# Kernel optimization log

Measured on AMD Instinct MI355X. Metric: run time of the kernel, lower is better.

Reference implementation:

```python
import jax, jax.numpy as jnp
import numpy as np

LN2 = float(np.log(2.0))
N_ATOMS = 100_000
N_PAIRS = 2_000_000
F = 64     # number_of_atom_features
R = 16     # number_of_radial_basis_functions
N_RES = 3


def setup_inputs() -> dict:
    key = jax.random.key(0)
    ks = jax.random.split(key, 16)
    s = 0.05
    inp = {
        "pair_indices": jax.random.randint(ks[0], (2, N_PAIRS), 0, N_ATOMS, dtype=jnp.int32),
        "f_ij": jax.random.normal(ks[1], (N_PAIRS, 1, R), dtype=jnp.float32),
        "d_ij": jax.random.uniform(ks[2], (N_PAIRS, 1), dtype=jnp.float32),
        "atomic_embedding": jax.random.normal(ks[3], (N_ATOMS, F), dtype=jnp.float32),
        # AttentionMask parameter G: [F, R]
        "G": jax.random.normal(ks[4], (F, R), dtype=jnp.float32),
        # interaction_i / interaction_j linear layers (stored as [in, out])
        "Wi": jax.random.normal(ks[5], (F, F), dtype=jnp.float32) * s,
        "bi": jnp.zeros((F,), dtype=jnp.float32),
        "Wj": jax.random.normal(ks[6], (F, F), dtype=jnp.float32) * s,
        "bj": jnp.zeros((F,), dtype=jnp.float32),
        # residual blocks, stacked over N_RES
        "res_W1": jax.random.normal(ks[7], (N_RES, F, F), dtype=jnp.float32) * s,
        "res_b1": jnp.zeros((N_RES, F), dtype=jnp.float32),
        "res_W2": jax.random.normal(ks[8], (N_RES, F, F), dtype=jnp.float32) * s,
        "res_b2": jnp.zeros((N_RES, F), dtype=jnp.float32),
        # process_v linear
        "Wv": jax.random.normal(ks[9], (F, F), dtype=jnp.float32) * s,
        "bv": jnp.zeros((F,), dtype=jnp.float32),
    }
    return inp


def reference(pair_indices, f_ij, d_ij, atomic_embedding,
              G, Wi, bi, Wj, bj, res_W1, res_b1, res_W2, res_b2, Wv, bv):
    idx_i, idx_j = pair_indices[0], pair_indices[1]
    f = f_ij.squeeze(1)                                  # [P, R]

    # ShiftedSoftplus on node embeddings
    x = jax.nn.softplus(atomic_embedding) - LN2          # [N, F]

    x_i_prime = jax.nn.softplus(x @ Wi + bi)             # [N, F]
    x_j_prime = jax.nn.softplus(x[idx_j] @ Wj + bj)      # [P, F] (gather)
    f_prime = f @ G.T                                    # [P, F] attention mask

    msg = x_j_prime * f_prime                            # [P, F]
    summed = jax.ops.segment_sum(msg, idx_i, num_segments=atomic_embedding.shape[0])

    v = x_i_prime + summed                               # [N, F]
    for l in range(res_W1.shape[0]):
        h = jax.nn.softplus(v @ res_W1[l] + res_b1[l])
        v = v + (h @ res_W2[l] + res_b2[l])
    return jax.nn.softplus(v) @ Wv + bv
```

## Files before the change

### kernel.cpp

```cpp
#include <hip/hip_runtime.h>
#include <math.h>

#define FDIM 64
#define RDIM 16
#define LN2F 0.69314718055994530942f
#define LTS 68
#define NBINR 14336
#define NCHUNK 64

typedef __bf16 bf8_t __attribute__((ext_vector_type(8)));
typedef float  f4_t  __attribute__((ext_vector_type(4)));

__device__ __forceinline__ float sp(float x) {
    return fmaxf(x, 0.0f) + __logf(1.0f + __expf(-fabsf(x)));
}

__global__ __launch_bounds__(256) void k_prep(
    const float* s0, const float* s1, const float* s2, const float* s3,
    const float* s4, const float* s5, const float* s6, const float* s7,
    const float* s8, __bf16* __restrict__ dst)
{
    const float* srcs[9] = {s0, s1, s2, s3, s4, s5, s6, s7, s8};
    const float* W = srcs[blockIdx.x];
    __bf16* d = dst + (size_t)blockIdx.x * 4096;
    for (int slot = threadIdx.x; slot < 512; slot += 256) {
        int f = slot >> 6, l = slot & 63;
        int kt = f >> 2, nt = f & 3;
        int row0 = kt * 32 + (l >> 4) * 8;
        int col = nt * 16 + (l & 15);
#pragma unroll
        for (int j = 0; j < 8; ++j)
            d[slot * 8 + j] = (__bf16)W[(row0 + j) * FDIM + col];
    }
}

__global__ __launch_bounds__(256) void k_hist2(
    const int* __restrict__ idx_i, int* __restrict__ Cmat,
    int P, int N, int nRange)
{
    __shared__ int h[NBINR];
    const int chunk = blockIdx.x / nRange;
    const int range = blockIdx.x % nRange;
    const int lo = range * NBINR;
    const int nb = min(NBINR, N - lo);
    for (int u = threadIdx.x; u < NBINR; u += 256) h[u] = 0;
    __syncthreads();

    const int chunkSz = (P + NCHUNK - 1) / NCHUNK;
    const int cs = chunk * chunkSz;
    const int ce = min(P, cs + chunkSz);
    int p = cs + threadIdx.x;
    for (; p + 768 < ce; p += 1024) {
        int i0 = idx_i[p];
        int i1 = idx_i[p + 256];
        int i2 = idx_i[p + 512];
        int i3 = idx_i[p + 768];
        unsigned u0 = (unsigned)(i0 - lo);
        unsigned u1 = (unsigned)(i1 - lo);
        unsigned u2 = (unsigned)(i2 - lo);
        unsigned u3 = (unsigned)(i3 - lo);
        if (u0 < (unsigned)nb) atomicAdd(&h[u0], 1);
        if (u1 < (unsigned)nb) atomicAdd(&h[u1], 1);
        if (u2 < (unsigned)nb) atomicAdd(&h[u2], 1);
        if (u3 < (unsigned)nb) atomicAdd(&h[u3], 1);
    }
    for (; p < ce; p += 256) {
        unsigned u = (unsigned)(idx_i[p] - lo);
        if (u < (unsigned)nb) atomicAdd(&h[u], 1);
    }
    __syncthreads();
    for (int u = threadIdx.x; u < nb; u += 256)
        Cmat[(size_t)chunk * N + lo + u] = h[u];
}

__global__ __launch_bounds__(256) void k_scanR(
    int* __restrict__ Cmat, int* __restrict__ tot, int N)
{
    const int bA = blockIdx.x * 512 + threadIdx.x;
    const int bB = bA + 256;
    const bool okA = bA < N, okB = bB < N;
    int runA = 0, runB = 0;
    for (int c = 0; c < NCHUNK; ++c) {
        const size_t base = (size_t)c * N;
        if (okA) { int val = Cmat[base + bA]; Cmat[base + bA] = runA; runA += val; }
        if (okB) { int val = Cmat[base + bB]; Cmat[base + bB] = runB; runB += val; }
    }
    if (okA) tot[bA] = runA;
    if (okB) tot[bB] = runB;
}

__device__ __forceinline__ void tile_in(float* T, const float* __restrict__ src,
                                        int a0, int rows, int lane)
{
#pragma unroll 4
    for (int i = 0; i < 16; ++i) {
        int r = i * 4 + (lane >> 4);
        int col = (lane & 15) * 4;
        float4 val = make_float4(0.f, 0.f, 0.f, 0.f);
        if (r < rows) val = *(const float4*)&src[(size_t)(a0 + r) * FDIM + col];
        *(float4*)&T[r * LTS + col] = val;
    }
}

__device__ __forceinline__ void build_a(const float* T, int lane, bool actLn2,
                                        bf8_t (&aF)[4][2])
{
    const int l15 = lane & 15, quad = lane >> 4;
#pragma unroll
    for (int mt = 0; mt < 4; ++mt) {
#pragma unroll
        for (int kt = 0; kt < 2; ++kt) {
            const float* rp = &T[(mt * 16 + l15) * LTS + kt * 32 + quad * 8];
            float4 u0 = *(const float4*)rp;
            float4 u1 = *(const float4*)(rp + 4);
            float e[8] = {u0.x, u0.y, u0.z, u0.w, u1.x, u1.y, u1.z, u1.w};
            bf8_t f;
#pragma unroll
            for (int j = 0; j < 8; ++j) {
                float t = actLn2 ? (sp(e[j]) - LN2F) : e[j];
                f[j] = (__bf16)t;
            }
            aF[mt][kt] = f;
        }
    }
}

__global__ __launch_bounds__(256) void k_atoms(
    const float* __restrict__ emb, const __bf16* __restrict__ wf,
    const float* __restrict__ bi, const float* __restrict__ bj,
    float* __restrict__ v, float* __restrict__ y, int N)
{
    __shared__ float tile[4][64 * LTS];
    const int lane = threadIdx.x & 63;
    const int wv = threadIdx.x >> 6;
    float* T = tile[wv];
    const int l15 = lane & 15, quad = lane >> 4;

    const bf8_t* wiF = (const bf8_t*)wf;
    const bf8_t* wjF = (const bf8_t*)(wf + 4096);
    bf8_t wi[2][4], wj[2][4];
#pragma unroll
    for (int kt = 0; kt < 2; ++kt)
#pragma unroll
        for (int nt = 0; nt < 4; ++nt) {
            wi[kt][nt] = wiF[(kt * 4 + nt) * 64 + lane];
            wj[kt][nt] = wjF[(kt * 4 + nt) * 64 + lane];
        }
    float biv[4], bjv[4];
#pragma unroll
    for (int nt = 0; nt < 4; ++nt) {
        biv[nt] = bi[nt * 16 + l15];
        bjv[nt] = bj[nt * 16 + l15];
    }

    const int nTiles = (N + 63) >> 6;
    for (int t = blockIdx.x * 4 + wv; t < nTiles; t += gridDim.x * 4) {
        const int a0 = t << 6;
        const int rows = min(64, N - a0);
        tile_in(T, emb, a0, rows, lane);
        bf8_t aF[4][2];
        build_a(T, lane, true, aF);
#pragma unroll
        for (int mt = 0; mt < 4; ++mt)
#pragma unroll
            for (int nt = 0; nt < 4; ++nt) {
                f4_t acc = {biv[nt], biv[nt], biv[nt], biv[nt]};
                acc = __builtin_amdgcn_mfma_f32_16x16x32_bf16(aF[mt][0], wi[0][nt], acc, 0, 0, 0);
                acc = __builtin_amdgcn_mfma_f32_16x16x32_bf16(aF[mt][1], wi[1][nt], acc, 0, 0, 0);
#pragma unroll
                for (int reg = 0; reg < 4; ++reg) {
                    int r = mt * 16 + quad * 4 + reg;
                    if (r < rows) v[(size_t)(a0 + r) * FDIM + nt * 16 + l15] = sp(acc[reg]);
                }
            }
#pragma unroll
        for (int mt = 0; mt < 4; ++mt)
#pragma unroll
            for (int nt = 0; nt < 4; ++nt) {
                f4_t acc = {bjv[nt], bjv[nt], bjv[nt], bjv[nt]};
                acc = __builtin_amdgcn_mfma_f32_16x16x32_bf16(aF[mt][0], wj[0][nt], acc, 0, 0, 0);
                acc = __builtin_amdgcn_mfma_f32_16x16x32_bf16(aF[mt][1], wj[1][nt], acc, 0, 0, 0);
#pragma unroll
                for (int reg = 0; reg < 4; ++reg) {
                    int r = mt * 16 + quad * 4 + reg;
                    if (r < rows) y[(size_t)(a0 + r) * FDIM + nt * 16 + l15] = sp(acc[reg]);
                }
            }
    }
}

__global__ __launch_bounds__(256) void k_post(
    const __bf16* __restrict__ wf,
    const float* __restrict__ rb1, const float* __restrict__ rb2,
    const float* __restrict__ bv,
    float* __restrict__ v, int N)
{
    __shared__ float tile[4][64 * LTS];
    const int lane = threadIdx.x & 63;
    const int wv = threadIdx.x >> 6;
    float* T = tile[wv];
    const int l15 = lane & 15, quad = lane >> 4;

    float b1v[3][4], b2v[3][4], bvv[4];
#pragma unroll
    for (int l = 0; l < 3; ++l)
#pragma unroll
        for (int nt = 0; nt < 4; ++nt) {
            b1v[l][nt] = rb1[l * FDIM + nt * 16 + l15];
            b2v[l][nt] = rb2[l * FDIM + nt * 16 + l15];
        }
#pragma unroll
    for (int nt = 0; nt < 4; ++nt) bvv[nt] = bv[nt * 16 + l15];

    const int nTiles = (N + 63) >> 6;
    for (int t = blockIdx.x * 4 + wv; t < nTiles; t += gridDim.x * 4) {
        const int a0 = t << 6;
        const int rows = min(64, N - a0);
        tile_in(T, v, a0, rows, lane);
        float vC[16][4];
#pragma unroll
        for (int mt = 0; mt < 4; ++mt)
#pragma unroll
            for (int nt = 0; nt < 4; ++nt)
#pragma unroll
                for (int reg = 0; reg < 4; ++reg)
                    vC[mt * 4 + nt][reg] =
                        T[(mt * 16 + quad * 4 + reg) * LTS + nt * 16 + l15];

        for (int l = 0; l < 3; ++l) {
            const bf8_t* w1f = (const bf8_t*)(wf + (size_t)(2 * l) * 4096);
            const bf8_t* w2f = (const bf8_t*)(wf + (size_t)(2 * l + 1) * 4096);
            bf8_t aF[4][2];
            build_a(T, lane, false, aF);
#pragma unroll
            for (int mt = 0; mt < 4; ++mt)
#pragma unroll
                for (int nt = 0; nt < 4; ++nt) {
                    f4_t acc = {b1v[l][nt], b1v[l][nt], b1v[l][nt], b1v[l][nt]};
                    acc = __builtin_amdgcn_mfma_f32_16x16x32_bf16(aF[mt][0], w1f[(0 * 4 + nt) * 64 + lane], acc, 0, 0, 0);
                    acc = __builtin_amdgcn_mfma_f32_16x16x32_bf16(aF[mt][1], w1f[(1 * 4 + nt) * 64 + lane], acc, 0, 0, 0);
#pragma unroll
                    for (int reg = 0; reg < 4; ++reg)
                        T[(mt * 16 + quad * 4 + reg) * LTS + nt * 16 + l15] = sp(acc[reg]);
                }
            bf8_t hF[4][2];
            build_a(T, lane, false, hF);
#pragma unroll
            for (int mt = 0; mt < 4; ++mt)
#pragma unroll
                for (int nt = 0; nt < 4; ++nt) {
                    f4_t acc = {b2v[l][nt], b2v[l][nt], b2v[l][nt], b2v[l][nt]};
                    acc = __builtin_amdgcn_mfma_f32_16x16x32_bf16(hF[mt][0], w2f[(0 * 4 + nt) * 64 + lane], acc, 0, 0, 0);
                    acc = __builtin_amdgcn_mfma_f32_16x16x32_bf16(hF[mt][1], w2f[(1 * 4 + nt) * 64 + lane], acc, 0, 0, 0);
#pragma unroll
                    for (int reg = 0; reg < 4; ++reg)
                        vC[mt * 4 + nt][reg] += acc[reg];
                }
            if (l < 2) {
#pragma unroll
                for (int mt = 0; mt < 4; ++mt)
#pragma unroll
                    for (int nt = 0; nt < 4; ++nt)
#pragma unroll
                        for (int reg = 0; reg < 4; ++reg)
                            T[(mt * 16 + quad * 4 + reg) * LTS + nt * 16 + l15] =
                                vC[mt * 4 + nt][reg];
            }
        }
#pragma unroll
        for (int mt = 0; mt < 4; ++mt)
#pragma unroll
            for (int nt = 0; nt < 4; ++nt)
#pragma unroll
                for (int reg = 0; reg < 4; ++reg)
                    T[(mt * 16 + quad * 4 + reg) * LTS + nt * 16 + l15] =
                        sp(vC[mt * 4 + nt][reg]);
        bf8_t fF[4][2];
        build_a(T, lane, false, fF);
        const bf8_t* wvf = (const bf8_t*)(wf + (size_t)6 * 4096);
#pragma unroll
        for (int mt = 0; mt < 4; ++mt)
#pragma unroll
            for (int nt = 0; nt < 4; ++nt) {
                f4_t acc = {bvv[nt], bvv[nt], bvv[nt], bvv[nt]};
                acc = __builtin_amdgcn_mfma_f32_16x16x32_bf16(fF[mt][0], wvf[(0 * 4 + nt) * 64 + lane], acc, 0, 0, 0);
                acc = __builtin_amdgcn_mfma_f32_16x16x32_bf16(fF[mt][1], wvf[(1 * 4 + nt) * 64 + lane], acc, 0, 0, 0);
#pragma unroll
                for (int reg = 0; reg < 4; ++reg) {
                    int r = mt * 16 + quad * 4 + reg;
                    if (r < rows) v[(size_t)(a0 + r) * FDIM + nt * 16 + l15] = acc[reg];
                }
            }
    }
}

__global__ __launch_bounds__(256) void k_scan_a(
    const int* __restrict__ cnt, int* __restrict__ part, int N)
{
    __shared__ int red[256];
    int b = blockIdx.x, t = threadIdx.x;
    int base = b * 1024 + t * 4;
    int s = 0;
#pragma unroll
    for (int i = 0; i < 4; ++i) { int a = base + i; if (a < N) s += cnt[a]; }
    red[t] = s; __syncthreads();
    for (int off = 128; off > 0; off >>= 1) {
        if (t < off) red[t] += red[t + off];
        __syncthreads();
    }
    if (t == 0) part[b] = red[0];
}

__global__ __launch_bounds__(256) void k_scan_b(int* __restrict__ part, int nPart)
{
    __shared__ int lds[256];
    int t = threadIdx.x;
    int base = t * 4;
    int v[4]; int s = 0;
#pragma unroll
    for (int i = 0; i < 4; ++i) { v[i] = (base + i < nPart) ? part[base + i] : 0; s += v[i]; }
    lds[t] = s; __syncthreads();
    int run = s;
    for (int off = 1; off < 256; off <<= 1) {
        int x = (t >= off) ? lds[t - off] : 0;
        __syncthreads();
        lds[t] += x;
        __syncthreads();
    }
    int excl = lds[t] - run;
#pragma unroll
    for (int i = 0; i < 4; ++i) { if (base + i < nPart) { part[base + i] = excl; excl += v[i]; } }
}

__global__ __launch_bounds__(256) void k_scan_c(
    const int* __restrict__ cnt, const int* __restrict__ part,
    int* __restrict__ start, int N, int P)
{
    __shared__ int lds[256];
    int b = blockIdx.x, t = threadIdx.x;
    int base = b * 1024 + t * 4;
    int v[4]; int s = 0;
#pragma unroll
    for (int i = 0; i < 4; ++i) { int a = base + i; v[i] = (a < N) ? cnt[a] : 0; s += v[i]; }
    lds[t] = s; __syncthreads();
    int run = s;
    for (int off = 1; off < 256; off <<= 1) {
        int x = (t >= off) ? lds[t - off] : 0;
        __syncthreads();
        lds[t] += x;
        __syncthreads();
    }
    int pre = part[b] + (lds[t] - run);
#pragma unroll
    for (int i = 0; i < 4; ++i) {
        int a = base + i;
        if (a < N) { start[a] = pre; pre += v[i]; }
    }
    if (b == 0 && t == 0) start[N] = P;
}

__global__ __launch_bounds__(256) void k_scatter2(
    const int* __restrict__ pidx, const int* __restrict__ Cmat,
    const int* __restrict__ start, int2* __restrict__ sorted,
    int P, int N, int nRange)
{
    __shared__ int cur[NBINR];
    const int chunk = blockIdx.x / nRange;
    const int range = blockIdx.x % nRange;
    const int lo = range * NBINR;
    const int nb = min(NBINR, N - lo);
    for (int u = threadIdx.x; u < nb; u += 256)
        cur[u] = start[lo + u] + Cmat[(size_t)chunk * N + lo + u];
    __syncthreads();

    const int chunkSz = (P + NCHUNK - 1) / NCHUNK;
    const int cs = chunk * chunkSz;
    const int ce = min(P, cs + chunkSz);
    int p = cs + threadIdx.x;
    for (; p + 768 < ce; p += 1024) {
        int i0 = pidx[p];
        int i1 = pidx[p + 256];
        int i2 = pidx[p + 512];
        int i3 = pidx[p + 768];
        int j0 = pidx[P + p];
        int j1 = pidx[P + p + 256];
        int j2 = pidx[P + p + 512];
        int j3 = pidx[P + p + 768];
        unsigned u0 = (unsigned)(i0 - lo);
        unsigned u1 = (unsigned)(i1 - lo);
        unsigned u2 = (unsigned)(i2 - lo);
        unsigned u3 = (unsigned)(i3 - lo);
        if (u0 < (unsigned)nb) { int pos = atomicAdd(&cur[u0], 1); sorted[pos] = make_int2(p, j0); }
        if (u1 < (unsigned)nb) { int pos = atomicAdd(&cur[u1], 1); sorted[pos] = make_int2(p + 256, j1); }
        if (u2 < (unsigned)nb) { int pos = atomicAdd(&cur[u2], 1); sorted[pos] = make_int2(p + 512, j2); }
        if (u3 < (unsigned)nb) { int pos = atomicAdd(&cur[u3], 1); sorted[pos] = make_int2(p + 768, j3); }
    }
    for (; p < ce; p += 256) {
        int i = pidx[p];
        unsigned u = (unsigned)(i - lo);
        if (u < (unsigned)nb) {
            int j = pidx[P + p];
            int pos = atomicAdd(&cur[u], 1);
            sorted[pos] = make_int2(p, j);
        }
    }
}

__global__ __launch_bounds__(256) void k_seg(
    const int2* __restrict__ sorted, const int* __restrict__ start,
    const float* __restrict__ f_ij, const float* __restrict__ G,
    const float* __restrict__ y, float* __restrict__ v, int N)
{
    const int c = threadIdx.x & 63;
    const int w = __builtin_amdgcn_readfirstlane((blockIdx.x << 2) | (threadIdx.x >> 6));
    const int nw = gridDim.x << 2;

    float g[16];
    {
        const float4* gp = (const float4*)(G + c * RDIM);
        float4 g0 = gp[0], g1 = gp[1], g2 = gp[2], g3 = gp[3];
        g[0] = g0.x;  g[1] = g0.y;  g[2] = g0.z;  g[3] = g0.w;
        g[4] = g1.x;  g[5] = g1.y;  g[6] = g1.z;  g[7] = g1.w;
        g[8] = g2.x;  g[9] = g2.y;  g[10] = g2.z; g[11] = g2.w;
        g[12] = g3.x; g[13] = g3.y; g[14] = g3.z; g[15] = g3.w;
    }

    for (int a = w; a < N; a += nw) {
        const int s = start[a], e = start[a + 1];
        float vold = v[(size_t)a * FDIM + c];
        float t[16];
#pragma unroll
        for (int r = 0; r < 16; ++r) t[r] = 0.0f;

        for (int base = s; base < e; base += 64) {
            const int nn = (e - base < 64) ? (e - base) : 64;
            const int li = (c < nn) ? c : (nn - 1);
            const int2 E = sorted[base + li];
            const int pk = E.x, jk = E.y;

            int k = 0;
            for (; k + 8 <= nn; k += 8) {
                int pp[8], jj[8];
#pragma unroll
                for (int u = 0; u < 8; ++u) {
                    pp[u] = __builtin_amdgcn_readlane(pk, k + u);
                    jj[u] = __builtin_amdgcn_readlane(jk, k + u);
                }
                float yv[8];
#pragma unroll
                for (int u = 0; u < 8; ++u)
                    yv[u] = y[(size_t)jj[u] * FDIM + c];
#pragma unroll
                for (int u = 0; u < 8; ++u) {
                    const float* f = f_ij + (size_t)pp[u] * RDIM;
#pragma unroll
                    for (int r = 0; r < 16; ++r) t[r] = fmaf(f[r], yv[u], t[r]);
                }
            }
            for (; k + 4 <= nn; k += 4) {
                int pp[4], jj[4];
#pragma unroll
                for (int u = 0; u < 4; ++u) {
                    pp[u] = __builtin_amdgcn_readlane(pk, k + u);
                    jj[u] = __builtin_amdgcn_readlane(jk, k + u);
                }
                float yv[4];
#pragma unroll
                for (int u = 0; u < 4; ++u)
                    yv[u] = y[(size_t)jj[u] * FDIM + c];
#pragma unroll
                for (int u = 0; u < 4; ++u) {
                    const float* f = f_ij + (size_t)pp[u] * RDIM;
#pragma unroll
                    for (int r = 0; r < 16; ++r) t[r] = fmaf(f[r], yv[u], t[r]);
                }
            }
            for (; k < nn; ++k) {
                const int p0 = __builtin_amdgcn_readlane(pk, k);
                const int j0 = __builtin_amdgcn_readlane(jk, k);
                float y0 = y[(size_t)j0 * FDIM + c];
                const float* f0 = f_ij + (size_t)p0 * RDIM;
#pragma unroll
                for (int r = 0; r < 16; ++r) t[r] = fmaf(f0[r], y0, t[r]);
            }
        }

        float acc0 = 0.f, acc1 = 0.f, acc2 = 0.f, acc3 = 0.f;
#pragma unroll
        for (int r = 0; r < 16; r += 4) {
            acc0 = fmaf(g[r + 0], t[r + 0], acc0);
            acc1 = fmaf(g[r + 1], t[r + 1], acc1);
            acc2 = fmaf(g[r + 2], t[r + 2], acc2);
            acc3 = fmaf(g[r + 3], t[r + 3], acc3);
        }
        v[(size_t)a * FDIM + c] = vold + (acc0 + acc1) + (acc2 + acc3);
    }
}

extern "C" void kernel_launch(void* const* d_in, const int* in_sizes, int n_in,
                              void* d_out, int out_size, void* d_ws, size_t ws_size,
                              hipStream_t stream)
{
    const int*   pidx = (const int*)d_in[0];
    const float* f_ij = (const float*)d_in[1];
    const float* emb  = (const float*)d_in[3];
    const float* G    = (const float*)d_in[4];
    const float* Wi   = (const float*)d_in[5];
    const float* bi   = (const float*)d_in[6];
    const float* Wj   = (const float*)d_in[7];
    const float* bj   = (const float*)d_in[8];
    const float* rW1  = (const float*)d_in[9];
    const float* rb1  = (const float*)d_in[10];
    const float* rW2  = (const float*)d_in[11];
    const float* rb2  = (const float*)d_in[12];
    const float* Wv   = (const float*)d_in[13];
    const float* bv   = (const float*)d_in[14];

    const int P = in_sizes[0] / 2;
    const int N = in_sizes[3] / FDIM;

    float* v = (float*)d_out;

    char* ws = (char*)d_ws;
    size_t off = 0;
    float*  y      = (float*)(ws + off);
    int*    Cmat   = (int*)(ws + off);    off += (size_t)N * FDIM * 4;
    int*    tot    = (int*)(ws + off);    off += (size_t)N * 4;
    int*    start  = (int*)(ws + off);    off += (size_t)(N + 1) * 4;
    off = (off + 15) & ~(size_t)15;
    int*    part   = (int*)(ws + off);    off += (size_t)4096 * 4;
    off = (off + 15) & ~(size_t)15;
    int2*   sorted = (int2*)(ws + off);   off += (size_t)P * 8;
    off = (off + 15) & ~(size_t)15;
    __bf16* wf     = (__bf16*)(ws + off); off += (size_t)9 * 4096 * 2;

    const int nRange = (N + NBINR - 1) / NBINR;
    const int nPart = (N + 1023) / 1024;
    const int nTiles = (N + 63) >> 6;
    const int gTiles = (nTiles + 3) / 4;

    dim3 blk(256);
    k_prep<<<9, blk, 0, stream>>>(Wi, Wj, rW1, rW2, rW1 + 4096, rW2 + 4096,
                                  rW1 + 8192, rW2 + 8192, Wv, wf);
    k_hist2<<<NCHUNK * nRange, blk, 0, stream>>>(pidx, Cmat, P, N, nRange);
    k_scanR<<<(N + 511) / 512, blk, 0, stream>>>(Cmat, tot, N);
    k_scan_a<<<nPart, blk, 0, stream>>>(tot, part, N);
    k_scan_b<<<1, blk, 0, stream>>>(part, nPart);
    k_scan_c<<<nPart, blk, 0, stream>>>(tot, part, start, N, P);
    k_scatter2<<<NCHUNK * nRange, blk, 0, stream>>>(pidx, Cmat, start, sorted, P, N, nRange);
    k_atoms<<<gTiles, blk, 0, stream>>>(emb, wf, bi, bj, v, y, N);
    k_seg<<<4096, blk, 0, stream>>>(sorted, start, f_ij, G, y, v, N);
    k_post<<<gTiles, blk, 0, stream>>>(wf + (size_t)2 * 4096, rb1, rb2, bv, v, N);
}
```

Baseline: 634.3 us.

## Pre-sort f_ij as fp16 during scatter and use fdot2 in segment kernel

The scatter kernel now writes each pair's radial features, converted to fp16, into the sorted order alongside its j index. The segment kernel can then read them contiguously instead of gathering f_ij rows at random. The segment kernel computes each pair's f·G dot product with packed fp16 dot2 instructions per channel, replacing the 16-wide accumulation followed by a G reduction. This trades extra per-channel dot work and fp16 precision loss for coalesced, halved f traffic. It also drops the 4x-unrolled scatter loop, and the scatter now has to read all f_ij in random-write order.

```diff
diff --git a/kernel.cpp b/kernel.cpp
--- a/kernel.cpp
+++ b/kernel.cpp
@@ -10,9 +10,18 @@
 
 typedef __bf16 bf8_t __attribute__((ext_vector_type(8)));
 typedef float  f4_t  __attribute__((ext_vector_type(4)));
+typedef _Float16 h2_t __attribute__((ext_vector_type(2)));
 
 __device__ __forceinline__ float sp(float x) {
     return fmaxf(x, 0.0f) + __logf(1.0f + __expf(-fabsf(x)));
+}
+
+__device__ __forceinline__ float fdot2f(h2_t a, h2_t b, float c) {
+#if __has_builtin(__builtin_amdgcn_fdot2)
+    return __builtin_amdgcn_fdot2(a, b, c, false);
+#else
+    return c + (float)a[0] * (float)b[0] + (float)a[1] * (float)b[1];
+#endif
 }
 
 __global__ __launch_bounds__(256) void k_prep(
@@ -360,8 +369,9 @@
 }
 
 __global__ __launch_bounds__(256) void k_scatter2(
-    const int* __restrict__ pidx, const int* __restrict__ Cmat,
-    const int* __restrict__ start, int2* __restrict__ sorted,
+    const int* __restrict__ pidx, const float* __restrict__ f_ij,
+    const int* __restrict__ Cmat, const int* __restrict__ start,
+    int* __restrict__ sortedJ, _Float16* __restrict__ sortedF,
     int P, int N, int nRange)
 {
     __shared__ int cur[NBINR];
@@ -376,123 +386,100 @@
     const int chunkSz = (P + NCHUNK - 1) / NCHUNK;
     const int cs = chunk * chunkSz;
     const int ce = min(P, cs + chunkSz);
-    int p = cs + threadIdx.x;
-    for (; p + 768 < ce; p += 1024) {
-        int i0 = pidx[p];
-        int i1 = pidx[p + 256];
-        int i2 = pidx[p + 512];
-        int i3 = pidx[p + 768];
-        int j0 = pidx[P + p];
-        int j1 = pidx[P + p + 256];
-        int j2 = pidx[P + p + 512];
-        int j3 = pidx[P + p + 768];
-        unsigned u0 = (unsigned)(i0 - lo);
-        unsigned u1 = (unsigned)(i1 - lo);
-        unsigned u2 = (unsigned)(i2 - lo);
-        unsigned u3 = (unsigned)(i3 - lo);
-        if (u0 < (unsigned)nb) { int pos = atomicAdd(&cur[u0], 1); sorted[pos] = make_int2(p, j0); }
-        if (u1 < (unsigned)nb) { int pos = atomicAdd(&cur[u1], 1); sorted[pos] = make_int2(p + 256, j1); }
-        if (u2 < (unsigned)nb) { int pos = atomicAdd(&cur[u2], 1); sorted[pos] = make_int2(p + 512, j2); }
-        if (u3 < (unsigned)nb) { int pos = atomicAdd(&cur[u3], 1); sorted[pos] = make_int2(p + 768, j3); }
-    }
-    for (; p < ce; p += 256) {
+    for (int p = cs + threadIdx.x; p < ce; p += 256) {
         int i = pidx[p];
         unsigned u = (unsigned)(i - lo);
         if (u < (unsigned)nb) {
             int j = pidx[P + p];
             int pos = atomicAdd(&cur[u], 1);
-            sorted[pos] = make_int2(p, j);
+            sortedJ[pos] = j;
+            const float4* fp = (const float4*)(f_ij + (size_t)p * RDIM);
+            float4 A = fp[0], B = fp[1], C4 = fp[2], D = fp[3];
+            h2_t hv[8];
+            hv[0] = h2_t{(_Float16)A.x, (_Float16)A.y};
+            hv[1] = h2_t{(_Float16)A.z, (_Float16)A.w};
+            hv[2] = h2_t{(_Float16)B.x, (_Float16)B.y};
+            hv[3] = h2_t{(_Float16)B.z, (_Float16)B.w};
+            hv[4] = h2_t{(_Float16)C4.x, (_Float16)C4.y};
+            hv[5] = h2_t{(_Float16)C4.z, (_Float16)C4.w};
+            hv[6] = h2_t{(_Float16)D.x, (_Float16)D.y};
+            hv[7] = h2_t{(_Float16)D.z, (_Float16)D.w};
+            _Float16* dst = sortedF + (size_t)pos * 16;
+            *(uint4*)dst = *(const uint4*)&hv[0];
+            *(uint4*)(dst + 8) = *(const uint4*)&hv[4];
         }
     }
 }
 
 __global__ __launch_bounds__(256) void k_seg(
-    const int2* __restrict__ sorted, const int* __restrict__ start,
-    const float* __restrict__ f_ij, const float* __restrict__ G,
+    const int* __restrict__ sortedJ, const _Float16* __restrict__ sortedF,
+    const int* __restrict__ start, const float* __restrict__ G,
     const float* __restrict__ y, float* __restrict__ v, int N)
 {
     const int c = threadIdx.x & 63;
     const int w = __builtin_amdgcn_readfirstlane((blockIdx.x << 2) | (threadIdx.x >> 6));
     const int nw = gridDim.x << 2;
 
-    float g[16];
+    h2_t g2[8];
     {
         const float4* gp = (const float4*)(G + c * RDIM);
-        float4 g0 = gp[0], g1 = gp[1], g2 = gp[2], g3 = gp[3];
-        g[0] = g0.x;  g[1] = g0.y;  g[2] = g0.z;  g[3] = g0.w;
-        g[4] = g1.x;  g[5] = g1.y;  g[6] = g1.z;  g[7] = g1.w;
-        g[8] = g2.x;  g[9] = g2.y;  g[10] = g2.z; g[11] = g2.w;
-        g[12] = g3.x; g[13] = g3.y; g[14] = g3.z; g[15] = g3.w;
+        float4 g0 = gp[0], g1 = gp[1], g2v = gp[2], g3 = gp[3];
+        g2[0] = h2_t{(_Float16)g0.x, (_Float16)g0.y};
+        g2[1] = h2_t{(_Float16)g0.z, (_Float16)g0.w};
+        g2[2] = h2_t{(_Float16)g1.x, (_Float16)g1.y};
+        g2[3] = h2_t{(_Float16)g1.z, (_Float16)g1.w};
+        g2[4] = h2_t{(_Float16)g2v.x, (_Float16)g2v.y};
+        g2[5] = h2_t{(_Float16)g2v.z, (_Float16)g2v.w};
+        g2[6] = h2_t{(_Float16)g3.x, (_Float16)g3.y};
+        g2[7] = h2_t{(_Float16)g3.z, (_Float16)g3.w};
     }
 
     for (int a = w; a < N; a += nw) {
-        const int s = start[a], e = start[a + 1];
+        const int s = __builtin_amdgcn_readfirstlane(start[a]);
+        const int e = __builtin_amdgcn_readfirstlane(start[a + 1]);
         float vold = v[(size_t)a * FDIM + c];
-        float t[16];
-#pragma unroll
-        for (int r = 0; r < 16; ++r) t[r] = 0.0f;
+        float acc0 = 0.f, acc1 = 0.f, acc2 = 0.f, acc3 = 0.f;
 
         for (int base = s; base < e; base += 64) {
             const int nn = (e - base < 64) ? (e - base) : 64;
             const int li = (c < nn) ? c : (nn - 1);
-            const int2 E = sorted[base + li];
-            const int pk = E.x, jk = E.y;
+            const int jkv = sortedJ[base + li];
 
             int k = 0;
             for (; k + 8 <= nn; k += 8) {
-                int pp[8], jj[8];
-#pragma unroll
-                for (int u = 0; u < 8; ++u) {
-                    pp[u] = __builtin_amdgcn_readlane(pk, k + u);
-                    jj[u] = __builtin_amdgcn_readlane(jk, k + u);
-                }
+                int jj[8];
+#pragma unroll
+                for (int u = 0; u < 8; ++u)
+                    jj[u] = __builtin_amdgcn_readlane(jkv, k + u);
                 float yv[8];
 #pragma unroll
                 for (int u = 0; u < 8; ++u)
                     yv[u] = y[(size_t)jj[u] * FDIM + c];
+                const h2_t* f2 = (const h2_t*)(sortedF + (size_t)(base + k) * 16);
 #pragma unroll
                 for (int u = 0; u < 8; ++u) {
-                    const float* f = f_ij + (size_t)pp[u] * RDIM;
-#pragma unroll
-                    for (int r = 0; r < 16; ++r) t[r] = fmaf(f[r], yv[u], t[r]);
+                    float d = 0.f;
+#pragma unroll
+                    for (int r = 0; r < 8; ++r)
+                        d = fdot2f(f2[u * 8 + r], g2[r], d);
+                    if ((u & 3) == 0) acc0 = fmaf(d, yv[u], acc0);
+                    else if ((u & 3) == 1) acc1 = fmaf(d, yv[u], acc1);
+                    else if ((u & 3) == 2) acc2 = fmaf(d, yv[u], acc2);
+                    else acc3 = fmaf(d, yv[u], acc3);
                 }
             }
-            for (; k + 4 <= nn; k += 4) {
-                int pp[4], jj[4];
-#pragma unroll
-                for (int u = 0; u < 4; ++u) {
-                    pp[u] = __builtin_amdgcn_readlane(pk, k + u);
-                    jj[u] = __builtin_amdgcn_readlane(jk, k + u);
-                }
-                float yv[4];
-#pragma unroll
-                for (int u = 0; u < 4; ++u)
-                    yv[u] = y[(size_t)jj[u] * FDIM + c];
-#pragma unroll
-                for (int u = 0; u < 4; ++u) {
-                    const float* f = f_ij + (size_t)pp[u] * RDIM;
-#pragma unroll
-                    for (int r = 0; r < 16; ++r) t[r] = fmaf(f[r], yv[u], t[r]);
-                }
-            }
             for (; k < nn; ++k) {
-                const int p0 = __builtin_amdgcn_readlane(pk, k);
-                const int j0 = __builtin_amdgcn_readlane(jk, k);
+                const int j0 = __builtin_amdgcn_readlane(jkv, k);
                 float y0 = y[(size_t)j0 * FDIM + c];
-                const float* f0 = f_ij + (size_t)p0 * RDIM;
-#pragma unroll
-                for (int r = 0; r < 16; ++r) t[r] = fmaf(f0[r], y0, t[r]);
+                const h2_t* f2 = (const h2_t*)(sortedF + (size_t)(base + k) * 16);
+                float d = 0.f;
+#pragma unroll
+                for (int r = 0; r < 8; ++r)
+                    d = fdot2f(f2[r], g2[r], d);
+                acc0 = fmaf(d, y0, acc0);
             }
         }
 
-        float acc0 = 0.f, acc1 = 0.f, acc2 = 0.f, acc3 = 0.f;
-#pragma unroll
-        for (int r = 0; r < 16; r += 4) {
-            acc0 = fmaf(g[r + 0], t[r + 0], acc0);
-            acc1 = fmaf(g[r + 1], t[r + 1], acc1);
-            acc2 = fmaf(g[r + 2], t[r + 2], acc2);
-            acc3 = fmaf(g[r + 3], t[r + 3], acc3);
-        }
         v[(size_t)a * FDIM + c] = vold + (acc0 + acc1) + (acc2 + acc3);
     }
 }
@@ -530,7 +517,9 @@
     off = (off + 15) & ~(size_t)15;
     int*    part   = (int*)(ws + off);    off += (size_t)4096 * 4;
     off = (off + 15) & ~(size_t)15;
-    int2*   sorted = (int2*)(ws + off);   off += (size_t)P * 8;
+    int*    sortedJ = (int*)(ws + off);   off += (size_t)P * 4;
+    off = (off + 63) & ~(size_t)63;
+    _Float16* sortedF = (_Float16*)(ws + off); off += (size_t)P * 16 * 2;
     off = (off + 15) & ~(size_t)15;
     __bf16* wf     = (__bf16*)(ws + off); off += (size_t)9 * 4096 * 2;
 
@@ -547,8 +536,9 @@
     k_scan_a<<<nPart, blk, 0, stream>>>(tot, part, N);
     k_scan_b<<<1, blk, 0, stream>>>(part, nPart);
     k_scan_c<<<nPart, blk, 0, stream>>>(tot, part, start, N, P);
-    k_scatter2<<<NCHUNK * nRange, blk, 0, stream>>>(pidx, Cmat, start, sorted, P, N, nRange);
+    k_scatter2<<<NCHUNK * nRange, blk, 0, stream>>>(pidx, f_ij, Cmat, start,
+                                                    sortedJ, sortedF, P, N, nRange);
     k_atoms<<<gTiles, blk, 0, stream>>>(emb, wf, bi, bj, v, y, N);
-    k_seg<<<4096, blk, 0, stream>>>(sorted, start, f_ij, G, y, v, N);
+    k_seg<<<4096, blk, 0, stream>>>(sortedJ, sortedF, start, G, y, v, N);
     k_post<<<gTiles, blk, 0, stream>>>(wf + (size_t)2 * 4096, rb1, rb2, bv, v, N);
 }
```

After: 711.9 us. 12.2% more time.
